# Kernel optimization log

Measured on AMD Instinct MI355X. Metric: run time of the kernel, lower is better.

Reference implementation:

```python
import jax, jax.numpy as jnp
import numpy as np

KERNEL_SIZE = 9
SIGMA_SPATIAL = 3.0
SIGMA_RANGE = 0.1
RADIUS = KERNEL_SIZE // 2


def setup_inputs() -> dict:
    key = jax.random.key(0)
    image = jax.random.uniform(key, (4096, 4096), dtype=jnp.float32)
    return {"image": image}


def reference(image):
    # Bilateral filter: out[i,j] = sum_w(spatial*range*window) / sum_w(spatial*range)
    H, W = image.shape
    r = RADIUS
    sigma_s_sq = 2.0 * SIGMA_SPATIAL ** 2
    sigma_r_sq = 2.0 * SIGMA_RANGE ** 2
    padded = jnp.pad(image, r, mode='reflect')  # (H+2r, W+2r)
    num = jnp.zeros_like(image)
    den = jnp.zeros_like(image)
    # Fixed 9x9 tap loop (81 iterations, unrolled by jit); fully vectorized over pixels.
    for dy in range(KERNEL_SIZE):
        for dx in range(KERNEL_SIZE):
            win = padded[dy:dy + H, dx:dx + W]  # (H, W) shifted window tap
            spatial_w = np.float32(np.exp(-((dx - r) ** 2 + (dy - r) ** 2) / sigma_s_sq))
            w = spatial_w * jnp.exp(-(win - image) ** 2 / sigma_r_sq)
            num = num + w * win
            den = den + w
    # Center tap weight is always 1, so den > 0 everywhere; plain divide matches torch branch.
    return num / den
```

## Files before the change

### kernel.cpp

```cpp
#include <hip/hip_runtime.h>

#define IMG_H 4096
#define IMG_W 4096
#define RAD 4
#define TSX 128
#define TSY 16
#define NPX 8
#define LROWS (TSY + 2*RAD)
#define LCOLS (TSX + 2*RAD)

__device__ __forceinline__ int reflect_idx(int i, int n) {
    i = (i < 0) ? -i : i;
    i = (i >= n) ? (2 * n - 2 - i) : i;
    return i;
}

__global__ __launch_bounds__(256, 4) void bilateral_kernel(const float* __restrict__ in,
                                                           float* __restrict__ out) {
    __shared__ float tile[LROWS * LCOLS];
    const int bx = blockIdx.x * TSX;
    const int by = blockIdx.y * TSY;
    const int tid = threadIdx.x;

    const bool interior = (blockIdx.x > 0) && (blockIdx.x < (int)gridDim.x - 1) &&
                          (blockIdx.y > 0) && (blockIdx.y < (int)gridDim.y - 1);
    if (interior) {
        const float* src = in + (size_t)(by - RAD) * IMG_W + (bx - RAD);
#pragma unroll
        for (int it = 0; it < 4; ++it) {
            int i = tid + it * 256;
            if (i < 816) {
                int row = i / 34;
                int col = i - row * 34;
                float4 q = *reinterpret_cast<const float4*>(src + row * IMG_W + col * 4);
                *reinterpret_cast<float4*>(&tile[row * 136 + col * 4]) = q;
            }
        }
    } else {
        for (int i = tid; i < LROWS * LCOLS; i += 256) {
            int ly = i / 136;
            int lx = i - ly * 136;
            int gy = reflect_idx(by + ly - RAD, IMG_H);
            int gx = reflect_idx(bx + lx - RAD, IMG_W);
            tile[ly * 136 + lx] = in[gy * IMG_W + gx];
        }
    }
    __syncthreads();

    const int tx = tid & 15;
    const int ty = tid >> 4;
    const int x0 = tx * NPX;

    constexpr float LOG2E = 1.4426950408889634f;
    constexpr float KR  = -50.0f * LOG2E;
    constexpr float S23 = 8388608.0f;
    constexpr float KRS = KR * S23;
    constexpr float NEG2KRS = -2.0f * KRS;
    constexpr float SCS = (-LOG2E / 18.0f) * S23;
    constexpr float BIAS = (127.0f - 0.04303f) * S23;

    float B[NPX], n[NPX], d[NPX];
    {
        float4 c0 = *reinterpret_cast<const float4*>(&tile[(ty + RAD) * 136 + x0 + 4]);
        float4 c1 = *reinterpret_cast<const float4*>(&tile[(ty + RAD) * 136 + x0 + 8]);
        B[0] = NEG2KRS * c0.x; B[1] = NEG2KRS * c0.y;
        B[2] = NEG2KRS * c0.z; B[3] = NEG2KRS * c0.w;
        B[4] = NEG2KRS * c1.x; B[5] = NEG2KRS * c1.y;
        B[6] = NEG2KRS * c1.z; B[7] = NEG2KRS * c1.w;
    }
#pragma unroll
    for (int p = 0; p < NPX; ++p) { n[p] = 0.f; d[p] = 0.f; }

    const float* rowp = &tile[ty * 136 + x0];

#pragma unroll 1
    for (int r = 0; r < 9; ++r) {
        const float4 q0 = *reinterpret_cast<const float4*>(rowp);
        const float4 q1 = *reinterpret_cast<const float4*>(rowp + 4);
        const float4 q2 = *reinterpret_cast<const float4*>(rowp + 8);
        const float4 q3 = *reinterpret_cast<const float4*>(rowp + 12);
        const float4 q4 = *reinterpret_cast<const float4*>(rowp + 16);
        rowp += 136;

        auto V = [&](int i) -> float {
            switch (i) {
                case 0:  return q0.x; case 1:  return q0.y; case 2:  return q0.z; case 3:  return q0.w;
                case 4:  return q1.x; case 5:  return q1.y; case 6:  return q1.z; case 7:  return q1.w;
                case 8:  return q2.x; case 9:  return q2.y; case 10: return q2.z; case 11: return q2.w;
                case 12: return q3.x; case 13: return q3.y; case 14: return q3.z; case 15: return q3.w;
                case 16: return q4.x; case 17: return q4.y; case 18: return q4.z; case 19: return q4.w;
            }
            return 0.f;
        };

        int e = r - 4;
        float syf = (float)(e * e) * SCS;
        const float sc0 = syf + (16.0f * SCS + BIAS);
        const float sc1 = syf + (9.0f  * SCS + BIAS);
        const float sc2 = syf + (4.0f  * SCS + BIAS);
        const float sc3 = syf + (1.0f  * SCS + BIAS);
        const float sc4 = syf + (0.0f  * SCS + BIAS);
        const float sc5 = sc3;
        const float sc6 = sc2;
        const float sc7 = sc1;
        const float sc8 = sc0;
        auto SCB = [&](int i) -> float {
            switch (i) {
                case 0: return sc0; case 1: return sc1; case 2: return sc2;
                case 3: return sc3; case 4: return sc4; case 5: return sc5;
                case 6: return sc6; case 7: return sc7; case 8: return sc8;
            }
            return 0.f;
        };

#pragma unroll
        for (int dx = 0; dx < 9; ++dx) {
            const float sc = SCB(dx);
#pragma unroll
            for (int p = 0; p < NPX; ++p) {
                float vv = V(dx + p);
                float t  = fmaf(KRS, vv, B[p]);
                float aa = fmaf(vv, t, sc);
                float w  = __int_as_float((int)aa);
                n[p] = fmaf(w, vv, n[p]);
                d[p] += w;
            }
        }
    }

    float4 o0, o1;
    o0.x = n[0] * __builtin_amdgcn_rcpf(d[0]);
    o0.y = n[1] * __builtin_amdgcn_rcpf(d[1]);
    o0.z = n[2] * __builtin_amdgcn_rcpf(d[2]);
    o0.w = n[3] * __builtin_amdgcn_rcpf(d[3]);
    o1.x = n[4] * __builtin_amdgcn_rcpf(d[4]);
    o1.y = n[5] * __builtin_amdgcn_rcpf(d[5]);
    o1.z = n[6] * __builtin_amdgcn_rcpf(d[6]);
    o1.w = n[7] * __builtin_amdgcn_rcpf(d[7]);

    float* orow = &out[(size_t)(by + ty) * IMG_W + bx + x0];
    *reinterpret_cast<float4*>(orow)     = o0;
    *reinterpret_cast<float4*>(orow + 4) = o1;
}

extern "C" void kernel_launch(void* const* d_in, const int* in_sizes, int n_in,
                              void* d_out, int out_size, void* d_ws, size_t ws_size,
                              hipStream_t stream) {
    const float* in = (const float*)d_in[0];
    float* out = (float*)d_out;
    dim3 grid(IMG_W / TSX, IMG_H / TSY);
    bilateral_kernel<<<grid, 256, 0, stream>>>(in, out);
}
```

Baseline: 235.2 us.

## Split thread pixels into two strided groups and replace float-to-int with shift exp trick

```diff
diff --git a/kernel.cpp b/kernel.cpp
--- a/kernel.cpp
+++ b/kernel.cpp
@@ -5,7 +5,6 @@
 #define RAD 4
 #define TSX 128
 #define TSY 16
-#define NPX 8
 #define LROWS (TSY + 2*RAD)
 #define LCOLS (TSX + 2*RAD)
 
@@ -49,46 +48,54 @@
 
     const int tx = tid & 15;
     const int ty = tid >> 4;
-    const int x0 = tx * NPX;
+    const int x0 = tx * 4;
 
     constexpr float LOG2E = 1.4426950408889634f;
-    constexpr float KR  = -50.0f * LOG2E;
-    constexpr float S23 = 8388608.0f;
-    constexpr float KRS = KR * S23;
+    constexpr float KR   = -50.0f * LOG2E;
+    constexpr float S15  = 32768.0f;
+    constexpr float KRS  = KR * S15;
     constexpr float NEG2KRS = -2.0f * KRS;
-    constexpr float SCS = (-LOG2E / 18.0f) * S23;
-    constexpr float BIAS = (127.0f - 0.04303f) * S23;
+    constexpr float SCS  = (-LOG2E / 18.0f) * S15;
+    constexpr float BIAS = (127.0f - 0.04303f) * S15 + 8388608.0f;
 
-    float B[NPX], n[NPX], d[NPX];
+    float B[8], n[8], d[8];
     {
-        float4 c0 = *reinterpret_cast<const float4*>(&tile[(ty + RAD) * 136 + x0 + 4]);
-        float4 c1 = *reinterpret_cast<const float4*>(&tile[(ty + RAD) * 136 + x0 + 8]);
-        B[0] = NEG2KRS * c0.x; B[1] = NEG2KRS * c0.y;
-        B[2] = NEG2KRS * c0.z; B[3] = NEG2KRS * c0.w;
-        B[4] = NEG2KRS * c1.x; B[5] = NEG2KRS * c1.y;
-        B[6] = NEG2KRS * c1.z; B[7] = NEG2KRS * c1.w;
+        const float* crow = &tile[(ty + RAD) * 136 + x0 + RAD];
+        float4 cA = *reinterpret_cast<const float4*>(crow);
+        float4 cB = *reinterpret_cast<const float4*>(crow + 64);
+        B[0] = NEG2KRS * cA.x; B[1] = NEG2KRS * cA.y;
+        B[2] = NEG2KRS * cA.z; B[3] = NEG2KRS * cA.w;
+        B[4] = NEG2KRS * cB.x; B[5] = NEG2KRS * cB.y;
+        B[6] = NEG2KRS * cB.z; B[7] = NEG2KRS * cB.w;
     }
 #pragma unroll
-    for (int p = 0; p < NPX; ++p) { n[p] = 0.f; d[p] = 0.f; }
+    for (int p = 0; p < 8; ++p) { n[p] = 0.f; d[p] = 0.f; }
 
     const float* rowp = &tile[ty * 136 + x0];
 
 #pragma unroll 1
     for (int r = 0; r < 9; ++r) {
-        const float4 q0 = *reinterpret_cast<const float4*>(rowp);
-        const float4 q1 = *reinterpret_cast<const float4*>(rowp + 4);
-        const float4 q2 = *reinterpret_cast<const float4*>(rowp + 8);
-        const float4 q3 = *reinterpret_cast<const float4*>(rowp + 12);
-        const float4 q4 = *reinterpret_cast<const float4*>(rowp + 16);
+        const float4 qa0 = *reinterpret_cast<const float4*>(rowp);
+        const float4 qa1 = *reinterpret_cast<const float4*>(rowp + 4);
+        const float4 qa2 = *reinterpret_cast<const float4*>(rowp + 8);
+        const float4 qb0 = *reinterpret_cast<const float4*>(rowp + 64);
+        const float4 qb1 = *reinterpret_cast<const float4*>(rowp + 68);
+        const float4 qb2 = *reinterpret_cast<const float4*>(rowp + 72);
         rowp += 136;
 
-        auto V = [&](int i) -> float {
+        auto VA = [&](int i) -> float {
             switch (i) {
-                case 0:  return q0.x; case 1:  return q0.y; case 2:  return q0.z; case 3:  return q0.w;
-                case 4:  return q1.x; case 5:  return q1.y; case 6:  return q1.z; case 7:  return q1.w;
-                case 8:  return q2.x; case 9:  return q2.y; case 10: return q2.z; case 11: return q2.w;
-                case 12: return q3.x; case 13: return q3.y; case 14: return q3.z; case 15: return q3.w;
-                case 16: return q4.x; case 17: return q4.y; case 18: return q4.z; case 19: return q4.w;
+                case 0:  return qa0.x; case 1:  return qa0.y; case 2:  return qa0.z; case 3:  return qa0.w;
+                case 4:  return qa1.x; case 5:  return qa1.y; case 6:  return qa1.z; case 7:  return qa1.w;
+                case 8:  return qa2.x; case 9:  return qa2.y; case 10: return qa2.z; case 11: return qa2.w;
+            }
+            return 0.f;
+        };
+        auto VB = [&](int i) -> float {
+            switch (i) {
+                case 0:  return qb0.x; case 1:  return qb0.y; case 2:  return qb0.z; case 3:  return qb0.w;
+                case 4:  return qb1.x; case 5:  return qb1.y; case 6:  return qb1.z; case 7:  return qb1.w;
+                case 8:  return qb2.x; case 9:  return qb2.y; case 10: return qb2.z; case 11: return qb2.w;
             }
             return 0.f;
         };
@@ -100,15 +107,11 @@
         const float sc2 = syf + (4.0f  * SCS + BIAS);
         const float sc3 = syf + (1.0f  * SCS + BIAS);
         const float sc4 = syf + (0.0f  * SCS + BIAS);
-        const float sc5 = sc3;
-        const float sc6 = sc2;
-        const float sc7 = sc1;
-        const float sc8 = sc0;
         auto SCB = [&](int i) -> float {
             switch (i) {
                 case 0: return sc0; case 1: return sc1; case 2: return sc2;
-                case 3: return sc3; case 4: return sc4; case 5: return sc5;
-                case 6: return sc6; case 7: return sc7; case 8: return sc8;
+                case 3: return sc3; case 4: return sc4; case 5: return sc3;
+                case 6: return sc2; case 7: return sc1; case 8: return sc0;
             }
             return 0.f;
         };
@@ -117,30 +120,40 @@
         for (int dx = 0; dx < 9; ++dx) {
             const float sc = SCB(dx);
 #pragma unroll
-            for (int p = 0; p < NPX; ++p) {
-                float vv = V(dx + p);
-                float t  = fmaf(KRS, vv, B[p]);
-                float aa = fmaf(vv, t, sc);
-                float w  = __int_as_float((int)aa);
-                n[p] = fmaf(w, vv, n[p]);
-                d[p] += w;
+            for (int p = 0; p < 4; ++p) {
+                {
+                    float vv = VA(dx + p);
+                    float t  = fmaf(KRS, vv, B[p]);
+                    float y  = fmaf(vv, t, sc);
+                    float w  = __int_as_float(__float_as_int(y) << 8);
+                    n[p] = fmaf(w, vv, n[p]);
+                    d[p] += w;
+                }
+                {
+                    float vv = VB(dx + p);
+                    float t  = fmaf(KRS, vv, B[p + 4]);
+                    float y  = fmaf(vv, t, sc);
+                    float w  = __int_as_float(__float_as_int(y) << 8);
+                    n[p + 4] = fmaf(w, vv, n[p + 4]);
+                    d[p + 4] += w;
+                }
             }
         }
     }
 
-    float4 o0, o1;
-    o0.x = n[0] * __builtin_amdgcn_rcpf(d[0]);
-    o0.y = n[1] * __builtin_amdgcn_rcpf(d[1]);
-    o0.z = n[2] * __builtin_amdgcn_rcpf(d[2]);
-    o0.w = n[3] * __builtin_amdgcn_rcpf(d[3]);
-    o1.x = n[4] * __builtin_amdgcn_rcpf(d[4]);
-    o1.y = n[5] * __builtin_amdgcn_rcpf(d[5]);
-    o1.z = n[6] * __builtin_amdgcn_rcpf(d[6]);
-    o1.w = n[7] * __builtin_amdgcn_rcpf(d[7]);
+    float4 oA, oB;
+    oA.x = n[0] * __builtin_amdgcn_rcpf(d[0]);
+    oA.y = n[1] * __builtin_amdgcn_rcpf(d[1]);
+    oA.z = n[2] * __builtin_amdgcn_rcpf(d[2]);
+    oA.w = n[3] * __builtin_amdgcn_rcpf(d[3]);
+    oB.x = n[4] * __builtin_amdgcn_rcpf(d[4]);
+    oB.y = n[5] * __builtin_amdgcn_rcpf(d[5]);
+    oB.z = n[6] * __builtin_amdgcn_rcpf(d[6]);
+    oB.w = n[7] * __builtin_amdgcn_rcpf(d[7]);
 
     float* orow = &out[(size_t)(by + ty) * IMG_W + bx + x0];
-    *reinterpret_cast<float4*>(orow)     = o0;
-    *reinterpret_cast<float4*>(orow + 4) = o1;
+    *reinterpret_cast<float4*>(orow)      = oA;
+    *reinterpret_cast<float4*>(orow + 64) = oB;
 }
 
 extern "C" void kernel_launch(void* const* d_in, const int* in_sizes, int n_in,
```

New measurement: 239.9 us. 1.02x slower.
